# Performance work log

Measured on AMD Instinct MI355X. Metric: run time of the kernel, lower is better.

## Reference

```python
import jax, jax.numpy as jnp
import numpy as np

C_IN, C_OUT, N_FILTERS = 64, 256, 16
CK = C_IN * N_FILTERS  # 1024
B, N, E = 2, 10000, 120000


def setup_inputs() -> dict:
    key = jax.random.key(0)
    k1, k2, k3, k4, k5, k6, k7, k8 = jax.random.split(key, 8)
    node_feats = jax.random.normal(k1, (B, N, C_IN), dtype=jnp.float32)
    node_positions = jax.random.uniform(k2, (B, N, 3), dtype=jnp.float32)
    edge_src = jax.random.randint(k3, (E,), 0, N, dtype=jnp.int32)
    edge_dst = jax.random.randint(k4, (E,), 0, N, dtype=jnp.int32)
    # original skips self-connections inside the adjacency list (self term is added separately)
    edge_src = jnp.where(edge_src == edge_dst, (edge_src + 1) % N, edge_src)
    W_dir = jax.random.normal(k5, (CK, 3), dtype=jnp.float32) * 0.05
    b_dir = jax.random.normal(k6, (CK,), dtype=jnp.float32) * 0.05
    W_feat = jax.random.normal(k7, (C_OUT, CK), dtype=jnp.float32) * 0.05
    b_feat = jax.random.normal(k8, (C_OUT,), dtype=jnp.float32) * 0.05
    return {"node_feats": node_feats, "node_positions": node_positions,
            "edge_src": edge_src, "edge_dst": edge_dst,
            "W_dir": W_dir, "b_dir": b_dir, "W_feat": W_feat, "b_feat": b_feat}


def reference(node_feats, node_positions, edge_src, edge_dst, W_dir, b_dir, W_feat, b_feat):
    n = node_feats.shape[1]
    # stacked features: node_feats repeated n_filters times along channels -> [B,N,CK]
    stacked = jnp.tile(node_feats, (1, 1, N_FILTERS))
    # per-edge direction: pos_other - pos_this  (this = dst node being aggregated into)
    d = node_positions[:, edge_src] - node_positions[:, edge_dst]  # [B,E,3]
    aff = jax.nn.relu(jnp.einsum('bed,kd->bek', d, W_dir) + b_dir)  # [B,E,CK]
    msg = stacked[:, edge_src] * aff                                 # [B,E,CK]
    agg = jax.vmap(lambda m: jax.ops.segment_sum(m, edge_dst, num_segments=n))(msg)  # [B,N,CK]
    # self contribution: direction = 0 -> relu(b_dir), gated own features
    agg = agg + stacked * jax.nn.relu(b_dir)
    out = jax.nn.relu(jnp.einsum('bnk,ok->bno', agg, W_feat) + b_feat)  # [B,N,c_out]
    return out
```

## Files before the change

kernel.cpp:

```cpp
#include <hip/hip_runtime.h>
#include <hip/hip_bf16.h>
#include <cstdint>
#include <cstddef>

constexpr int BATCH = 2;
constexpr int C_IN  = 64;
constexpr int CK    = 1024;
constexpr int C_OUT = 256;
constexpr int CHUNK = 32;

using bf16x8 = __attribute__((ext_vector_type(8))) short;
using f32x4  = __attribute__((ext_vector_type(4))) float;

#define GLOAD_LDS16(g, s) \
    __builtin_amdgcn_global_load_lds((const __attribute__((address_space(1))) void*)(g), \
                                     (__attribute__((address_space(3))) void*)(s), 16, 0, 0)

__global__ void hist_kernel(const int* __restrict__ dst, int* __restrict__ counts, int E) {
    int e = blockIdx.x * blockDim.x + threadIdx.x;
    if (e < E) atomicAdd(&counts[dst[e]], 1);
}

__global__ __launch_bounds__(1024)
void scan_kernel(const int* __restrict__ counts, int* __restrict__ offsets, int n) {
    __shared__ int wsum[16];
    __shared__ int carry_s;
    const int t = threadIdx.x;
    const int lane = t & 63;
    const int w = t >> 6;
    if (t == 0) carry_s = 0;
    __syncthreads();
    const int nch = (n + 1023) >> 10;
    for (int c = 0; c < nch; ++c) {
        const int idx = (c << 10) + t;
        const int v = (idx < n) ? counts[idx] : 0;
        int x = v;
        #pragma unroll
        for (int off = 1; off < 64; off <<= 1) {
            int y = __shfl_up(x, off, 64);
            if (lane >= off) x += y;
        }
        if (lane == 63) wsum[w] = x;
        __syncthreads();
        int wpre = 0, total = 0;
        #pragma unroll
        for (int i = 0; i < 16; ++i) {
            const int s = wsum[i];
            if (i < w) wpre += s;
            total += s;
        }
        const int carry = carry_s;
        if (idx < n) offsets[idx] = carry + wpre + (x - v);
        __syncthreads();
        if (t == 0) carry_s = carry + total;
    }
    if (t == 0) offsets[n] = carry_s;
}

__global__ void scatter_kernel(const int* __restrict__ dst, const int* __restrict__ src,
                               const int* __restrict__ offsets,
                               int* __restrict__ cursors, int* __restrict__ sorted_src, int E) {
    int e = blockIdx.x * blockDim.x + threadIdx.x;
    if (e < E) {
        const int d = dst[e];
        const int p = atomicAdd(&cursors[d], 1);
        sorted_src[offsets[d] + p] = src[e];
    }
}

__global__ __launch_bounds__(256)
void prep_kernel(const float* __restrict__ Wf, __hip_bfloat16* __restrict__ Wb,
                 const float* __restrict__ W_dir, const float* __restrict__ b_dir,
                 float4* __restrict__ Wp) {
    const int id = blockIdx.x * 256 + threadIdx.x;
    const int i = id * 4;
    const float4 v = *reinterpret_cast<const float4*>(Wf + i);
    __hip_bfloat162 a, b;
    a.x = __float2bfloat16(v.x); a.y = __float2bfloat16(v.y);
    b.x = __float2bfloat16(v.z); b.y = __float2bfloat16(v.w);
    *reinterpret_cast<__hip_bfloat162*>(Wb + i)     = a;
    *reinterpret_cast<__hip_bfloat162*>(Wb + i + 2) = b;
    if (id < CK)
        Wp[id] = make_float4(W_dir[id * 3 + 0], W_dir[id * 3 + 1], W_dir[id * 3 + 2], b_dir[id]);
}

__global__ __launch_bounds__(256)
void agg_kernel(const float* __restrict__ feats, const float* __restrict__ pos,
                const int* __restrict__ sorted_src, const int* __restrict__ offsets,
                const float4* __restrict__ Wp,
                __hip_bfloat16* __restrict__ agg, int N) {
    __shared__ float  feats_s[BATCH][CHUNK][C_IN];
    __shared__ float4 dir_s[BATCH][CHUNK];
    __shared__ int    sh_s[CHUNK];

    const int n = blockIdx.x;
    const int t = threadIdx.x;
    const int c0 = (2 * t) & 63;

    float4 wv[4];
    wv[0] = Wp[2 * t];       wv[1] = Wp[2 * t + 1];
    wv[2] = Wp[2 * t + 512]; wv[3] = Wp[2 * t + 513];

    float cx[BATCH], cy[BATCH], cz[BATCH];
    #pragma unroll
    for (int b = 0; b < BATCH; ++b) {
        const float* pb = pos + ((size_t)b * N + n) * 3;
        cx[b] = pb[0]; cy[b] = pb[1]; cz[b] = pb[2];
    }

    float acc[BATCH][4] = {};
    const int beg = offsets[n], end = offsets[n + 1];

    for (int j0 = beg; j0 < end; j0 += CHUNK) {
        const int cnt = min(CHUNK, end - j0);
        if (t < cnt) {
            const int s = sorted_src[j0 + t];
            sh_s[t] = s;
            #pragma unroll
            for (int b = 0; b < BATCH; ++b) {
                const float* ps = pos + ((size_t)b * N + s) * 3;
                dir_s[b][t] = make_float4(ps[0] - cx[b], ps[1] - cy[b], ps[2] - cz[b], 0.f);
            }
        }
        __syncthreads();
        #pragma unroll
        for (int b = 0; b < BATCH; ++b) {
            const float* fb = feats + (size_t)b * N * C_IN;
            for (int idx = t; idx < cnt * C_IN; idx += 256) {
                const int e = idx >> 6, ch = idx & 63;
                feats_s[b][e][ch] = fb[(size_t)sh_s[e] * C_IN + ch];
            }
        }
        __syncthreads();
        #pragma unroll
        for (int b = 0; b < BATCH; ++b) {
            for (int j = 0; j < cnt; ++j) {
                const float4 d = dir_s[b][j];
                const float2 f = *reinterpret_cast<const float2*>(&feats_s[b][j][c0]);
                #pragma unroll
                for (int u = 0; u < 4; ++u) {
                    const float a = fmaxf(fmaf(d.x, wv[u].x,
                                         fmaf(d.y, wv[u].y,
                                         fmaf(d.z, wv[u].z, wv[u].w))), 0.f);
                    acc[b][u] += ((u & 1) ? f.y : f.x) * a;
                }
            }
        }
        __syncthreads();
    }

    #pragma unroll
    for (int b = 0; b < BATCH; ++b) {
        const float2 fs = *reinterpret_cast<const float2*>(
            feats + ((size_t)b * N + n) * C_IN + c0);
        #pragma unroll
        for (int u = 0; u < 4; ++u)
            acc[b][u] += ((u & 1) ? fs.y : fs.x) * fmaxf(wv[u].w, 0.f);
        __hip_bfloat16* dst = agg + ((size_t)b * N + n) * CK;
        __hip_bfloat162 v01, v23;
        v01.x = __float2bfloat16(acc[b][0]); v01.y = __float2bfloat16(acc[b][1]);
        v23.x = __float2bfloat16(acc[b][2]); v23.y = __float2bfloat16(acc[b][3]);
        *reinterpret_cast<__hip_bfloat162*>(dst + 2 * t)       = v01;
        *reinterpret_cast<__hip_bfloat162*>(dst + 2 * t + 512) = v23;
    }
}

__global__ __launch_bounds__(256)
void gemm_kernel(const __hip_bfloat16* __restrict__ agg, const __hip_bfloat16* __restrict__ W,
                 const float* __restrict__ bf, float* __restrict__ out, int M) {
    __shared__ __hip_bfloat16 As[64 * 64];
    __shared__ __hip_bfloat16 Bs[64 * 64];
    const int t    = threadIdx.x;
    const int lane = t & 63;
    const int w    = t >> 6;
    const int q    = lane & 15;
    const int h    = lane >> 4;
    const int r0   = blockIdx.x * 64;
    const int c0   = blockIdx.y * 64;

    const int lrow    = lane >> 3;
    const int kschunk = (lane & 7) ^ lrow;

    f32x4 acc[2][2];
    #pragma unroll
    for (int mi = 0; mi < 2; ++mi)
        #pragma unroll
        for (int nj = 0; nj < 2; ++nj)
            #pragma unroll
            for (int r = 0; r < 4; ++r) acc[mi][nj][r] = 0.f;

    for (int k0 = 0; k0 < CK; k0 += 64) {
        #pragma unroll
        for (int i2 = 0; i2 < 2; ++i2) {
            const int seg = i2 * 4 + w;
            const int row = seg * 8 + lrow;
            const __hip_bfloat16* gA = agg + (size_t)(r0 + row) * CK + k0 + 8 * kschunk;
            const __hip_bfloat16* gB = W   + (size_t)(c0 + row) * CK + k0 + 8 * kschunk;
            GLOAD_LDS16(gA, As + seg * 512);
            GLOAD_LDS16(gB, Bs + seg * 512);
        }
        __syncthreads();

        #pragma unroll
        for (int kk = 0; kk < 2; ++kk) {
            bf16x8 af[2], bfr[2];
            #pragma unroll
            for (int mi = 0; mi < 2; ++mi) {
                const int row = (w >> 1) * 32 + mi * 16 + q;
                const int ch  = (kk * 4 + h) ^ (row & 7);
                af[mi] = *reinterpret_cast<const bf16x8*>(As + row * 64 + ch * 8);
            }
            #pragma unroll
            for (int nj = 0; nj < 2; ++nj) {
                const int row = (w & 1) * 32 + nj * 16 + q;
                const int ch  = (kk * 4 + h) ^ (row & 7);
                bfr[nj] = *reinterpret_cast<const bf16x8*>(Bs + row * 64 + ch * 8);
            }
            #pragma unroll
            for (int mi = 0; mi < 2; ++mi)
                #pragma unroll
                for (int nj = 0; nj < 2; ++nj)
                    acc[mi][nj] = __builtin_amdgcn_mfma_f32_16x16x32_bf16(
                        af[mi], bfr[nj], acc[mi][nj], 0, 0, 0);
        }
        __syncthreads();
    }

    #pragma unroll
    for (int mi = 0; mi < 2; ++mi) {
        #pragma unroll
        for (int nj = 0; nj < 2; ++nj) {
            const int col  = c0 + (w & 1) * 32 + nj * 16 + q;
            const float bias = bf[col];
            #pragma unroll
            for (int r = 0; r < 4; ++r) {
                const int row = r0 + (w >> 1) * 32 + mi * 16 + h * 4 + r;
                if (row < M)
                    out[(size_t)row * C_OUT + col] = fmaxf(acc[mi][nj][r] + bias, 0.f);
            }
        }
    }
}

extern "C" void kernel_launch(void* const* d_in, const int* in_sizes, int n_in,
                              void* d_out, int out_size, void* d_ws, size_t ws_size,
                              hipStream_t stream) {
    const float* feats  = (const float*)d_in[0];
    const float* pos    = (const float*)d_in[1];
    const int*   esrc   = (const int*)d_in[2];
    const int*   edst   = (const int*)d_in[3];
    const float* W_dir  = (const float*)d_in[4];
    const float* b_dir  = (const float*)d_in[5];
    const float* W_feat = (const float*)d_in[6];
    const float* b_feat = (const float*)d_in[7];
    float* out = (float*)d_out;

    const int N = in_sizes[1] / (BATCH * 3);
    const int E = in_sizes[2];
    const int M = BATCH * N;
    const int MBLK = (M + 63) / 64;
    const int M_pad = MBLK * 64;

    char* ws = (char*)d_ws;
    size_t off = 0;
    auto alignup = [&](size_t a) { off = (off + a - 1) & ~(a - 1); };

    __hip_bfloat16* agg = (__hip_bfloat16*)(ws + off); off += (size_t)M_pad * CK * sizeof(__hip_bfloat16);
    alignup(256);
    __hip_bfloat16* Wb  = (__hip_bfloat16*)(ws + off); off += (size_t)C_OUT * CK * sizeof(__hip_bfloat16);
    alignup(256);
    float4* Wp = (float4*)(ws + off); off += (size_t)CK * sizeof(float4);
    alignup(256);
    int* counts  = (int*)(ws + off); off += (size_t)N * sizeof(int);
    int* cursors = (int*)(ws + off); off += (size_t)N * sizeof(int);
    alignup(256);
    int* offsets = (int*)(ws + off); off += (size_t)(N + 1) * sizeof(int);
    alignup(256);
    int* sorted_src = (int*)(ws + off); off += (size_t)E * sizeof(int);

    hipMemsetAsync(counts, 0, (size_t)2 * N * sizeof(int), stream);
    hist_kernel<<<dim3((E + 255) / 256), dim3(256), 0, stream>>>(edst, counts, E);
    scan_kernel<<<dim3(1), dim3(1024), 0, stream>>>(counts, offsets, N);
    scatter_kernel<<<dim3((E + 255) / 256), dim3(256), 0, stream>>>(edst, esrc, offsets, cursors, sorted_src, E);
    prep_kernel<<<dim3(C_OUT * CK / 1024), dim3(256), 0, stream>>>(W_feat, Wb, W_dir, b_dir, Wp);
    agg_kernel<<<dim3(N), dim3(256), 0, stream>>>(feats, pos, sorted_src, offsets, Wp, agg, N);
    gemm_kernel<<<dim3(MBLK, C_OUT / 64), dim3(256), 0, stream>>>(agg, Wb, b_feat, out, M);
}
```

Measured before the change: 177.1 us.

## Double-buffer GEMM LDS, vectorize feature gather, unroll edge loop, widen scan

Several changes land together. The GEMM now stages the next K tile into a second LDS buffer while the current one is consumed by MFMAs, which removes one sync per step. The aggregation kernel gathers neighbor features with float4 loads, pads edge chunks to multiples of four using zeroed direction and feature entries, and unrolls the edge loop by four. The scan processes ten elements per thread per pass, cutting the number of serial block iterations. The double-buffered GEMM relies on its sync placement to avoid read/write races on the LDS buffers.

```diff
diff --git a/kernel.cpp b/kernel.cpp
--- a/kernel.cpp
+++ b/kernel.cpp
@@ -23,36 +23,50 @@
 
 __global__ __launch_bounds__(1024)
 void scan_kernel(const int* __restrict__ counts, int* __restrict__ offsets, int n) {
-    __shared__ int wsum[16];
+    __shared__ int wtot_s[16];
     __shared__ int carry_s;
     const int t = threadIdx.x;
     const int lane = t & 63;
     const int w = t >> 6;
     if (t == 0) carry_s = 0;
     __syncthreads();
-    const int nch = (n + 1023) >> 10;
-    for (int c = 0; c < nch; ++c) {
-        const int idx = (c << 10) + t;
-        const int v = (idx < n) ? counts[idx] : 0;
-        int x = v;
-        #pragma unroll
-        for (int off = 1; off < 64; off <<= 1) {
-            int y = __shfl_up(x, off, 64);
-            if (lane >= off) x += y;
-        }
-        if (lane == 63) wsum[w] = x;
-        __syncthreads();
-        int wpre = 0, total = 0;
+    for (int base = 0; base < n; base += 10240) {
+        int v[10], ex[10];
+        #pragma unroll
+        for (int g = 0; g < 10; ++g) {
+            const int idx = base + w * 640 + g * 64 + lane;
+            v[g] = (idx < n) ? counts[idx] : 0;
+        }
+        int run = 0;
+        #pragma unroll
+        for (int g = 0; g < 10; ++g) {
+            int x = v[g];
+            #pragma unroll
+            for (int off = 1; off < 64; off <<= 1) {
+                int y = __shfl_up(x, off, 64);
+                if (lane >= off) x += y;
+            }
+            ex[g] = run + x - v[g];
+            run += __shfl(x, 63, 64);
+        }
+        if (lane == 63) wtot_s[w] = run;
+        __syncthreads();
+        int wpre = 0, tot = 0;
         #pragma unroll
         for (int i = 0; i < 16; ++i) {
-            const int s = wsum[i];
+            const int s = wtot_s[i];
             if (i < w) wpre += s;
-            total += s;
+            tot += s;
         }
         const int carry = carry_s;
-        if (idx < n) offsets[idx] = carry + wpre + (x - v);
-        __syncthreads();
-        if (t == 0) carry_s = carry + total;
+        #pragma unroll
+        for (int g = 0; g < 10; ++g) {
+            const int idx = base + w * 640 + g * 64 + lane;
+            if (idx < n) offsets[idx] = carry + wpre + ex[g];
+        }
+        __syncthreads();
+        if (t == 0) carry_s = carry + tot;
+        __syncthreads();
     }
     if (t == 0) offsets[n] = carry_s;
 }
@@ -112,7 +126,8 @@
     const int beg = offsets[n], end = offsets[n + 1];
 
     for (int j0 = beg; j0 < end; j0 += CHUNK) {
-        const int cnt = min(CHUNK, end - j0);
+        const int cnt  = min(CHUNK, end - j0);
+        const int cnt4 = (cnt + 3) & ~3;
         if (t < cnt) {
             const int s = sorted_src[j0 + t];
             sh_s[t] = s;
@@ -121,28 +136,36 @@
                 const float* ps = pos + ((size_t)b * N + s) * 3;
                 dir_s[b][t] = make_float4(ps[0] - cx[b], ps[1] - cy[b], ps[2] - cz[b], 0.f);
             }
+        } else if (t < cnt4) {
+            dir_s[0][t] = make_float4(0.f, 0.f, 0.f, 0.f);
+            dir_s[1][t] = make_float4(0.f, 0.f, 0.f, 0.f);
         }
         __syncthreads();
         #pragma unroll
         for (int b = 0; b < BATCH; ++b) {
             const float* fb = feats + (size_t)b * N * C_IN;
-            for (int idx = t; idx < cnt * C_IN; idx += 256) {
-                const int e = idx >> 6, ch = idx & 63;
-                feats_s[b][e][ch] = fb[(size_t)sh_s[e] * C_IN + ch];
-            }
-        }
-        __syncthreads();
-        #pragma unroll
-        for (int b = 0; b < BATCH; ++b) {
-            for (int j = 0; j < cnt; ++j) {
-                const float4 d = dir_s[b][j];
-                const float2 f = *reinterpret_cast<const float2*>(&feats_s[b][j][c0]);
+            for (int idx = t; idx < cnt4 * 16; idx += 256) {
+                const int e = idx >> 4, q = idx & 15;
+                float4 v = make_float4(0.f, 0.f, 0.f, 0.f);
+                if (e < cnt) v = *reinterpret_cast<const float4*>(fb + (size_t)sh_s[e] * C_IN + q * 4);
+                *reinterpret_cast<float4*>(&feats_s[b][e][q * 4]) = v;
+            }
+        }
+        __syncthreads();
+        for (int j = 0; j < cnt4; j += 4) {
+            #pragma unroll
+            for (int jj = 0; jj < 4; ++jj) {
                 #pragma unroll
-                for (int u = 0; u < 4; ++u) {
-                    const float a = fmaxf(fmaf(d.x, wv[u].x,
-                                         fmaf(d.y, wv[u].y,
-                                         fmaf(d.z, wv[u].z, wv[u].w))), 0.f);
-                    acc[b][u] += ((u & 1) ? f.y : f.x) * a;
+                for (int b = 0; b < BATCH; ++b) {
+                    const float4 d = dir_s[b][j + jj];
+                    const float2 f = *reinterpret_cast<const float2*>(&feats_s[b][j + jj][c0]);
+                    #pragma unroll
+                    for (int u = 0; u < 4; ++u) {
+                        const float a = fmaxf(fmaf(d.x, wv[u].x,
+                                             fmaf(d.y, wv[u].y,
+                                             fmaf(d.z, wv[u].z, wv[u].w))), 0.f);
+                        acc[b][u] = fmaf((u & 1) ? f.y : f.x, a, acc[b][u]);
+                    }
                 }
             }
         }
@@ -168,8 +191,8 @@
 __global__ __launch_bounds__(256)
 void gemm_kernel(const __hip_bfloat16* __restrict__ agg, const __hip_bfloat16* __restrict__ W,
                  const float* __restrict__ bf, float* __restrict__ out, int M) {
-    __shared__ __hip_bfloat16 As[64 * 64];
-    __shared__ __hip_bfloat16 Bs[64 * 64];
+    __shared__ __hip_bfloat16 As[2][64 * 64];
+    __shared__ __hip_bfloat16 Bs[2][64 * 64];
     const int t    = threadIdx.x;
     const int lane = t & 63;
     const int w    = t >> 6;
@@ -189,17 +212,22 @@
             #pragma unroll
             for (int r = 0; r < 4; ++r) acc[mi][nj][r] = 0.f;
 
-    for (int k0 = 0; k0 < CK; k0 += 64) {
+    auto stage = [&](int buf, int k0) {
         #pragma unroll
         for (int i2 = 0; i2 < 2; ++i2) {
             const int seg = i2 * 4 + w;
             const int row = seg * 8 + lrow;
-            const __hip_bfloat16* gA = agg + (size_t)(r0 + row) * CK + k0 + 8 * kschunk;
-            const __hip_bfloat16* gB = W   + (size_t)(c0 + row) * CK + k0 + 8 * kschunk;
-            GLOAD_LDS16(gA, As + seg * 512);
-            GLOAD_LDS16(gB, Bs + seg * 512);
-        }
-        __syncthreads();
+            GLOAD_LDS16(agg + (size_t)(r0 + row) * CK + k0 + 8 * kschunk, &As[buf][seg * 512]);
+            GLOAD_LDS16(W   + (size_t)(c0 + row) * CK + k0 + 8 * kschunk, &Bs[buf][seg * 512]);
+        }
+    };
+
+    stage(0, 0);
+    __syncthreads();
+
+    for (int ks = 0; ks < 16; ++ks) {
+        const int cur = ks & 1;
+        if (ks < 15) stage(cur ^ 1, (ks + 1) * 64);
 
         #pragma unroll
         for (int kk = 0; kk < 2; ++kk) {
@@ -208,13 +236,13 @@
             for (int mi = 0; mi < 2; ++mi) {
                 const int row = (w >> 1) * 32 + mi * 16 + q;
                 const int ch  = (kk * 4 + h) ^ (row & 7);
-                af[mi] = *reinterpret_cast<const bf16x8*>(As + row * 64 + ch * 8);
+                af[mi] = *reinterpret_cast<const bf16x8*>(&As[cur][row * 64 + ch * 8]);
             }
             #pragma unroll
             for (int nj = 0; nj < 2; ++nj) {
                 const int row = (w & 1) * 32 + nj * 16 + q;
                 const int ch  = (kk * 4 + h) ^ (row & 7);
-                bfr[nj] = *reinterpret_cast<const bf16x8*>(Bs + row * 64 + ch * 8);
+                bfr[nj] = *reinterpret_cast<const bf16x8*>(&Bs[cur][row * 64 + ch * 8]);
             }
             #pragma unroll
             for (int mi = 0; mi < 2; ++mi)
```

Result: slower. 189.6 us (+7.1%).
